# Kernel tuning notes

Hardware: AMD Instinct MI355X
Metric: run time of the kernel (lower is better)

Reference implementation:

```python
import jax, jax.numpy as jnp
import numpy as np

N = 50000        # nodes
E = 800000       # edges per edge set (avg degree 16)
IN_DIM = 128
NHID = 128
OUT_DIM = 64


def _dgcn(x, ei, w=None):
    # DGCNConv: symmetric-normalized weighted scatter-add (no self loops, no learned weight)
    src, dst = ei[0], ei[1]
    ww = jnp.ones(src.shape[0], x.dtype) if w is None else w
    deg = jax.ops.segment_sum(ww, src, num_segments=N)
    dinv = jnp.where(deg > 0, jax.lax.rsqrt(jnp.maximum(deg, 1e-30)), 0.0)
    norm = dinv[src] * ww * dinv[dst]                    # [E]
    return jax.ops.segment_sum(x[src] * norm[:, None], dst, num_segments=N)


def _digcn(x, W, b, ei, w):
    # DIGCNConv: x @ W then edge-weighted scatter-add (weights precomputed), + bias
    xw = x @ W                                           # [N, out]
    src, dst = ei[0], ei[1]
    agg = jax.ops.segment_sum(xw[src] * w[:, None], dst, num_segments=N)
    return agg + b


def setup_inputs() -> dict:
    key = jax.random.key(0)
    ks = jax.random.split(key, 32)
    def edges(k):
        return jax.random.randint(k, (2, E), 0, N, dtype=jnp.int32)
    def w(k, shape, s=0.05):
        return jax.random.normal(k, shape, dtype=jnp.float32) * s
    inp = {
        "x": jax.random.normal(ks[0], (N, IN_DIM), dtype=jnp.float32),
        "edge_index": edges(ks[1]),
        "edge_in": edges(ks[2]),
        "in_w": jax.random.uniform(ks[3], (E,), dtype=jnp.float32),
        "edge_out": edges(ks[4]),
        "out_w": jax.random.uniform(ks[5], (E,), dtype=jnp.float32),
        "edge_index_ib": edges(ks[6]),
        "edge_weight_ib": jax.random.uniform(ks[7], (E,), dtype=jnp.float32),
        "edge_index2_ib": edges(ks[8]),
        "edge_weight2_ib": jax.random.uniform(ks[9], (E,), dtype=jnp.float32),
        # lin1 / lin2 (no bias), torch Linear convention W: [out, in]
        "lin1_w": w(ks[10], (NHID, IN_DIM)),
        "lin2_w": w(ks[11], (OUT_DIM, NHID)),
        # InceptionBlock 1: Linear(in->nhid) + two DIGCNConv(in->nhid)
        "ib1_ln_w": w(ks[12], (NHID, IN_DIM)),
        "ib1_ln_b": w(ks[13], (NHID,)),
        "ib1_c1_w": w(ks[14], (IN_DIM, NHID)),
        "ib1_c1_b": w(ks[15], (NHID,)),
        "ib1_c2_w": w(ks[16], (IN_DIM, NHID)),
        "ib1_c2_b": w(ks[17], (NHID,)),
        # InceptionBlock 2: nhid -> nhid
        "ib2_ln_w": w(ks[18], (NHID, NHID)),
        "ib2_ln_b": w(ks[19], (NHID,)),
        "ib2_c1_w": w(ks[20], (NHID, NHID)),
        "ib2_c1_b": w(ks[21], (NHID,)),
        "ib2_c2_w": w(ks[22], (NHID, NHID)),
        "ib2_c2_b": w(ks[23], (NHID,)),
        # Conv1d(2*nhid -> nhid, k=1) == pointwise linear: [nhid, 2*nhid]
        "conv1_w": w(ks[24], (NHID, 2 * NHID)),
        "conv1_b": w(ks[25], (NHID,)),
    }
    return inp


def reference(x, edge_index, edge_in, in_w, edge_out, out_w,
              edge_index_ib, edge_weight_ib, edge_index2_ib, edge_weight2_ib,
              lin1_w, lin2_w,
              ib1_ln_w, ib1_ln_b, ib1_c1_w, ib1_c1_b, ib1_c2_w, ib1_c2_b,
              ib2_ln_w, ib2_ln_b, ib2_c1_w, ib2_c1_b, ib2_c2_w, ib2_c2_b,
              conv1_w, conv1_b):
    # --- sym branch 1 (uses original sym edge_index) ---
    symx = x @ lin1_w.T
    symx = (_dgcn(symx, edge_index)
            + _dgcn(symx, edge_in, in_w)
            + _dgcn(symx, edge_out, out_w))
    # --- InceptionBlock 1 ---
    x0 = x @ ib1_ln_w.T + ib1_ln_b
    x1 = _digcn(x, ib1_c1_w, ib1_c1_b, edge_index_ib, edge_weight_ib)
    x2 = _digcn(x, ib1_c2_w, ib1_c2_b, edge_index2_ib, edge_weight2_ib)
    h = x0 + x1 + x2
    # cat + Conv1d(k=1) + relu  (dropout = identity in eval mode)
    h = jnp.concatenate([h, symx], axis=-1)              # [N, 2*nhid]
    h = jax.nn.relu(h @ conv1_w.T + conv1_b)
    # --- InceptionBlock 2 ---
    x0 = h @ ib2_ln_w.T + ib2_ln_b
    x1 = _digcn(h, ib2_c1_w, ib2_c1_b, edge_index_ib, edge_weight_ib)
    x2 = _digcn(h, ib2_c2_w, ib2_c2_b, edge_index2_ib, edge_weight2_ib)
    h = jax.nn.relu(x0 + x1 + x2)
    # --- final sym branch: NOTE edge_index was reassigned to edge_index_tuple[0] ---
    symx = h @ lin2_w.T
    out = (_dgcn(symx, edge_index_ib)
           + _dgcn(symx, edge_in, in_w)
           + _dgcn(symx, edge_out, out_w))
    return out
```

## Files before the change

### kernel.cpp

```cpp
#include <hip/hip_runtime.h>


static inline int cdiv(int a, int b) { return (a + b - 1) / b; }

struct __align__(8) TmpE { ushort s, d; float w; };

using bf16x8 = __attribute__((ext_vector_type(8))) short;
using f32x4  = __attribute__((ext_vector_type(4))) float;

constexpr int NCH  = 64;
constexpr int NCHH = 32;
constexpr int NW   = 25600;
constexpr int RNG  = 25000;
constexpr int AGS  = 384;

__device__ __forceinline__ float b2f(uint u)  { return __uint_as_float(u << 16); }
__device__ __forceinline__ float b2fh(uint u) { return __uint_as_float(u & 0xFFFF0000u); }
__device__ __forceinline__ ushort f2b(float f) {
  uint u = __float_as_uint(f);
  return (ushort)((u + 0x7FFFu + ((u >> 16) & 1u)) >> 16);
}
__device__ __forceinline__ uint pk2(float a, float b) {
  return (uint)f2b(a) | ((uint)f2b(b) << 16);
}
__device__ __forceinline__ uint pkent(uint s, float w) {
  return s | ((uint)f2b(w) << 16);
}


struct HistArgs {
  const int* ik[2];
  const int* fk[2]; const float* fw[2];
  uint* pint; float* pf32; int N, CH, E;
};

__global__ __launch_bounds__(1024) void k_hist(HistArgs a) {
  const int y = blockIdx.y, chunk = blockIdx.x;
  __shared__ uint h[NW];
  int e1 = min(a.E, (chunk + 1) * a.CH);
  if (y < 2) {
    const int* __restrict__ key = a.ik[y];
    for (int i = threadIdx.x; i < NW; i += 1024) h[i] = 0;
    __syncthreads();
    for (int e = chunk * a.CH + threadIdx.x; e < e1; e += 1024) {
      uint idx = (uint)key[e];
      atomicAdd(&h[idx >> 1], 1u << ((idx & 1) << 4));
    }
    __syncthreads();
    uint* out = a.pint + ((size_t)y * NCHH + chunk) * NW;
    for (int i = threadIdx.x; i < NW; i += 1024) out[i] = h[i];
  } else {
    const int job = (y - 2) >> 1, range = (y - 2) & 1;
    const int* __restrict__ key = a.fk[job];
    const float* __restrict__ w = a.fw[job];
    float* hf = (float*)h;
    for (int i = threadIdx.x; i < RNG; i += 1024) hf[i] = 0.0f;
    __syncthreads();
    const int base = range * RNG, hi = min(a.N, base + RNG);
    for (int e = chunk * a.CH + threadIdx.x; e < e1; e += 1024) {
      int s = key[e];
      if (s >= base && s < hi) atomicAdd(&hf[s - base], w[e]);
    }
    __syncthreads();
    float* out = a.pf32 + ((size_t)job * NCHH + chunk) * a.N;
    for (int i = threadIdx.x; i < hi - base; i += 1024) out[base + i] = hf[i];
  }
}


struct B1Jobs { const int* src[5]; const int* dst[5]; const float* w[5]; };

__global__ __launch_bounds__(256) void k_b1count(B1Jobs jobs, uint* __restrict__ bcnt,
                                                 int CH, int E) {
  const int chunk = blockIdx.x, set = blockIdx.y;
  const int* __restrict__ dst = jobs.dst[set];
  __shared__ uint h[256];
  h[threadIdx.x] = 0;
  __syncthreads();
  int e1 = min(E, (chunk + 1) * CH);
  for (int e = chunk * CH + threadIdx.x; e < e1; e += 256)
    atomicAdd(&h[((uint)dst[e]) >> 8], 1u);
  __syncthreads();
  bcnt[((size_t)set * NCH + chunk) * 256 + threadIdx.x] = h[threadIdx.x];
}

__global__ __launch_bounds__(1024) void k_scanfin(
    const uint* __restrict__ bcnt, uint* __restrict__ bpos, uint* __restrict__ bbase,
    const uint* __restrict__ pint, const float* __restrict__ pf32,
    float* __restrict__ dinv, int N, int E) {
  if (blockIdx.y == 0) {
    if (blockIdx.x >= 5) return;
    const int set = blockIdx.x;
    constexpr int CELLS = NCH * 256;
    constexpr int PER = CELLS / 1024;
    __shared__ uint lds[CELLS];
    __shared__ uint psum[1024];
    for (int i = threadIdx.x; i < CELLS; i += 1024) {
      int b = i / NCH, c = i % NCH;
      lds[i] = bcnt[((size_t)set * NCH + c) * 256 + b];
    }
    __syncthreads();
    uint s = 0;
#pragma unroll
    for (int k = 0; k < PER; k++) s += lds[threadIdx.x * PER + k];
    psum[threadIdx.x] = s;
    __syncthreads();
    for (int d = 1; d < 1024; d <<= 1) {
      uint t = (threadIdx.x >= d) ? psum[threadIdx.x - d] : 0;
      __syncthreads();
      psum[threadIdx.x] += t;
      __syncthreads();
    }
    uint run = threadIdx.x ? psum[threadIdx.x - 1] : 0;
#pragma unroll
    for (int k = 0; k < PER; k++) {
      uint v = lds[threadIdx.x * PER + k];
      lds[threadIdx.x * PER + k] = run;
      run += v;
    }
    __syncthreads();
    for (int i = threadIdx.x; i < CELLS; i += 1024) {
      int b = i / NCH, c = i % NCH;
      bpos[((size_t)set * NCH + c) * 256 + b] = lds[i];
      if (c == 0) bbase[(size_t)set * 257 + b] = lds[i];
    }
    if (threadIdx.x == 0) bbase[(size_t)set * 257 + 256] = (uint)E;
  } else {
    int n = blockIdx.x * 1024 + threadIdx.x;
    if (n >= N) return;
    const int wd = n >> 1, sh = (n & 1) << 4;
    uint s_sym = 0, s_ib = 0;
    float din = 0.0f, dout = 0.0f;
#pragma unroll
    for (int c = 0; c < NCHH; c++) {
      s_sym += (pint[((size_t)0 * NCHH + c) * NW + wd] >> sh) & 0xFFFFu;
      s_ib  += (pint[((size_t)1 * NCHH + c) * NW + wd] >> sh) & 0xFFFFu;
      din   += pf32[((size_t)0 * NCHH + c) * N + n];
      dout  += pf32[((size_t)1 * NCHH + c) * N + n];
    }
    dinv[(size_t)0 * N + n] = s_sym ? rsqrtf((float)s_sym) : 0.0f;
    dinv[(size_t)1 * N + n] = din  > 0.0f ? rsqrtf(din)  : 0.0f;
    dinv[(size_t)2 * N + n] = dout > 0.0f ? rsqrtf(dout) : 0.0f;
    dinv[(size_t)3 * N + n] = s_ib ? rsqrtf((float)s_ib) : 0.0f;
  }
}

__global__ __launch_bounds__(256) void k_b1scatter(B1Jobs jobs, const uint* __restrict__ bpos,
                                                   TmpE* __restrict__ tmp, int CH, int E) {
  const int chunk = blockIdx.x, set = blockIdx.y;
  const int* __restrict__ src = jobs.src[set];
  const int* __restrict__ dst = jobs.dst[set];
  const float* __restrict__ w = jobs.w[set];
  TmpE* __restrict__ tset = tmp + (size_t)set * E;
  __shared__ uint cur[256];
  cur[threadIdx.x] = bpos[((size_t)set * NCH + chunk) * 256 + threadIdx.x];
  __syncthreads();
  int e1 = min(E, (chunk + 1) * CH);
  for (int e = chunk * CH + threadIdx.x; e < e1; e += 256) {
    uint d = (uint)dst[e];
    uint pos = atomicAdd(&cur[d >> 8], 1u);
    TmpE t;
    t.s = (ushort)src[e];
    t.d = (ushort)d;
    t.w = w ? w[e] : 1.0f;
    tset[pos] = t;
  }
}


struct B2Job { const float* dinv; uint* entA; uint* entB; int raw; };
struct B2Jobs { B2Job j[5]; };

struct PrepArgs {
  const float *x; ushort *xb; int nx;
  const float *ln, *c1, *c2, *lin1, *convw; ushort *Wf1;
  const float *lnb, *c1b, *c2b, *convb; float *Bf1;
  const float *ln2, *c12, *c22; ushort *Wst2;
  const float *ln2b, *c1b2, *c2b2; float *bias2;
  const float *lin2; ushort *Wlin2;
};

__global__ __launch_bounds__(256) void k_b2prep(
    B2Jobs jobs, const TmpE* __restrict__ tmp, const uint* __restrict__ bbase,
    int* __restrict__ rptr, int N, int E, int NBK, PrepArgs a) {
  const int y = blockIdx.y;
  if (y < 5) {
    if (blockIdx.x >= NBK) return;
    const int b = blockIdx.x, set = y;
    const B2Job jb = jobs.j[set];
    const TmpE* __restrict__ tset = tmp + (size_t)set * E;
    const uint base = bbase[(size_t)set * 257 + b];
    const uint end  = bbase[(size_t)set * 257 + b + 1];
    __shared__ uint cnt[256];
    __shared__ uint scn[256];
    cnt[threadIdx.x] = 0;
    __syncthreads();
    for (uint t = base + threadIdx.x; t < end; t += 256)
      atomicAdd(&cnt[tset[t].d & 255], 1u);
    __syncthreads();
    uint v = cnt[threadIdx.x];
    scn[threadIdx.x] = v;
    __syncthreads();
    for (int d = 1; d < 256; d <<= 1) {
      uint t2 = (threadIdx.x >= d) ? scn[threadIdx.x - d] : 0;
      __syncthreads();
      scn[threadIdx.x] += t2;
      __syncthreads();
    }
    const uint ex = scn[threadIdx.x] - v;
    const int node0 = b << 8;
    int* rp = rptr + (size_t)set * (N + 1);
    if (node0 + threadIdx.x < N) rp[node0 + threadIdx.x] = (int)(base + ex);
    if (b == 0 && threadIdx.x == 0) rp[N] = (int)bbase[(size_t)set * 257 + 256];
    __syncthreads();
    cnt[threadIdx.x] = base + ex;
    __syncthreads();
    for (uint t = base + threadIdx.x; t < end; t += 256) {
      TmpE e = tset[t];
      uint pos = atomicAdd(&cnt[e.d & 255], 1u);
      float wA = jb.raw ? e.w : jb.dinv[e.s] * e.w * jb.dinv[e.d];
      jb.entA[pos] = pkent(e.s, wA);
      if (jb.entB) jb.entB[pos] = pkent(e.s, jb.dinv[e.s] * jb.dinv[e.d]);
    }
  } else if (y == 5) {
    int i = (blockIdx.x * 256 + threadIdx.x) * 16;
    if (i < a.nx) {
#pragma unroll
      for (int q = 0; q < 4; q++) {
        float4 v = *reinterpret_cast<const float4*>(a.x + i + q * 4);
        ushort4 o;
        o.x = f2b(v.x); o.y = f2b(v.y); o.z = f2b(v.z); o.w = f2b(v.w);
        *reinterpret_cast<ushort4*>(a.xb + i + q * 4) = o;
      }
    }
  } else {
    const int x = blockIdx.x;
    if (x < 256) {
      int id = x * 256 + threadIdx.x;
      int m = id >> 9, k = id & 511;
      int p = k >> 7, kk = k & 127;
      float s = 0.0f;
      if (p == 0) {
        for (int j = 0; j < 128; j++) s = fmaf(a.ln[j * 128 + kk], a.convw[m * 256 + j], s);
      } else if (p == 1) {
        for (int j = 0; j < 128; j++) s = fmaf(a.c1[kk * 128 + j], a.convw[m * 256 + j], s);
      } else if (p == 2) {
        for (int j = 0; j < 128; j++) s = fmaf(a.c2[kk * 128 + j], a.convw[m * 256 + j], s);
      } else {
        for (int j = 0; j < 128; j++) s = fmaf(a.lin1[j * 128 + kk], a.convw[m * 256 + 128 + j], s);
      }
      a.Wf1[m * 512 + k] = f2b(s);
    } else if (x < 448) {
      int id = (x - 256) * 256 + threadIdx.x;
      int m = id / 384, k = id % 384;
      int p = k >> 7, kk = k & 127;
      float v = (p == 0) ? a.ln2[m * 128 + kk]
              : (p == 1) ? a.c12[kk * 128 + m] : a.c22[kk * 128 + m];
      a.Wst2[m * 384 + k] = f2b(v);
    } else if (x < 456) {
      int i = ((x - 448) * 256 + threadIdx.x) * 4;
      if (i < 64 * 128) {
        float4 v = *reinterpret_cast<const float4*>(a.lin2 + i);
        ushort4 o;
        o.x = f2b(v.x); o.y = f2b(v.y); o.z = f2b(v.z); o.w = f2b(v.w);
        *reinterpret_cast<ushort4*>(a.Wlin2 + i) = o;
      }
    } else if (x == 456) {
      if (threadIdx.x < 128) {
        int m = threadIdx.x;
        float s = a.convb[m];
        for (int j = 0; j < 128; j++)
          s = fmaf(a.lnb[j] + a.c1b[j] + a.c2b[j], a.convw[m * 256 + j], s);
        a.Bf1[m] = s;
      }
    } else if (x == 457) {
      if (threadIdx.x < 128)
        a.bias2[threadIdx.x] = a.ln2b[threadIdx.x] + a.c1b2[threadIdx.x] + a.c2b2[threadIdx.x];
    }
  }
}

template <int K, int K1, int LDA2, int BN, bool RELU>
__global__ __launch_bounds__(256) void k_mgemm(
    const ushort* A1, const ushort* A2,
    const ushort* __restrict__ Wt, const float* __restrict__ bias,
    ushort* C, int N) {
  constexpr int WAVES_N = BN / 64;
  constexpr int WAVES_M = 4 / WAVES_N;
  constexpr int TM = 64 / WAVES_M;
  constexpr int MF = TM / 16;
  constexpr int NF = 4;

  const int tid = threadIdx.x;
  const int wid = tid >> 6;
  const int lane = tid & 63;
  const int lr = lane & 15;
  const int g = lane >> 4;
  const int wm = wid / WAVES_N;
  const int wnn = wid % WAVES_N;
  const int row0 = blockIdx.x * 64 + wm * TM;
  const int col0 = wnn * 64;

  f32x4 acc[MF][NF];
#pragma unroll
  for (int mi = 0; mi < MF; mi++)
#pragma unroll
    for (int ni = 0; ni < NF; ni++)
#pragma unroll
      for (int r = 0; r < 4; r++) acc[mi][ni][r] = 0.0f;

#pragma unroll
  for (int kk = 0; kk < K / 32; kk++) {
    const ushort* A; int lda, kofs;
    if (kk * 32 < K1) { A = A1; lda = 128; kofs = kk * 32; }
    else              { A = A2; lda = LDA2; kofs = kk * 32 - K1; }
    bf16x8 af[MF], bfr[NF];
#pragma unroll
    for (int mi = 0; mi < MF; mi++)
      af[mi] = *reinterpret_cast<const bf16x8*>(
          A + (size_t)(row0 + mi * 16 + lr) * lda + kofs + 8 * g);
#pragma unroll
    for (int ni = 0; ni < NF; ni++)
      bfr[ni] = *reinterpret_cast<const bf16x8*>(
          Wt + (size_t)(col0 + ni * 16 + lr) * K + kk * 32 + 8 * g);
#pragma unroll
    for (int mi = 0; mi < MF; mi++)
#pragma unroll
      for (int ni = 0; ni < NF; ni++)
        acc[mi][ni] = __builtin_amdgcn_mfma_f32_16x16x32_bf16(
            af[mi], bfr[ni], acc[mi][ni], 0, 0, 0);
  }

  float bv[NF];
#pragma unroll
  for (int ni = 0; ni < NF; ni++) bv[ni] = bias ? bias[col0 + ni * 16 + lr] : 0.0f;

#pragma unroll
  for (int mi = 0; mi < MF; mi++)
#pragma unroll
    for (int r = 0; r < 4; r++) {
      int row = row0 + mi * 16 + g * 4 + r;
      if (row >= N) continue;
#pragma unroll
      for (int ni = 0; ni < NF; ni++) {
        float v = acc[mi][ni][r] + bv[ni];
        if (RELU) v = fmaxf(v, 0.0f);
        C[(size_t)row * BN + col0 + ni * 16 + lr] = f2b(v);
      }
    }
}

__global__ __launch_bounds__(256) void k_mgemm23(
    const ushort* A1, const ushort* A2,
    const ushort* __restrict__ Wt, const float* __restrict__ bias,
    const ushort* __restrict__ W2, ushort* __restrict__ B64, int N) {
  constexpr int K = 384, K1 = 128;
  const int tid = threadIdx.x;
  const int wid = tid >> 6;
  const int lane = tid & 63;
  const int lr = lane & 15;
  const int g = lane >> 4;
  const int wm = wid >> 1;
  const int wnn = wid & 1;
  const int brow = blockIdx.x * 64;
  const int row0 = brow + wm * 32;
  const int col0 = wnn * 64;

  __shared__ ushort h2t[64][136];

  f32x4 acc[2][4];
#pragma unroll
  for (int mi = 0; mi < 2; mi++)
#pragma unroll
    for (int ni = 0; ni < 4; ni++)
#pragma unroll
      for (int r = 0; r < 4; r++) acc[mi][ni][r] = 0.0f;

#pragma unroll
  for (int kk = 0; kk < K / 32; kk++) {
    const ushort* A; int lda, kofs;
    if (kk * 32 < K1) { A = A1; lda = 128; kofs = kk * 32; }
    else              { A = A2; lda = AGS; kofs = kk * 32 - K1; }
    bf16x8 af[2], bfr[4];
#pragma unroll
    for (int mi = 0; mi < 2; mi++)
      af[mi] = *reinterpret_cast<const bf16x8*>(
          A + (size_t)(row0 + mi * 16 + lr) * lda + kofs + 8 * g);
#pragma unroll
    for (int ni = 0; ni < 4; ni++)
      bfr[ni] = *reinterpret_cast<const bf16x8*>(
          Wt + (size_t)(col0 + ni * 16 + lr) * K + kk * 32 + 8 * g);
#pragma unroll
    for (int mi = 0; mi < 2; mi++)
#pragma unroll
      for (int ni = 0; ni < 4; ni++)
        acc[mi][ni] = __builtin_amdgcn_mfma_f32_16x16x32_bf16(
            af[mi], bfr[ni], acc[mi][ni], 0, 0, 0);
  }

  float bv[4];
#pragma unroll
  for (int ni = 0; ni < 4; ni++) bv[ni] = bias[col0 + ni * 16 + lr];

#pragma unroll
  for (int mi = 0; mi < 2; mi++)
#pragma unroll
    for (int r = 0; r < 4; r++) {
      int lrow = wm * 32 + mi * 16 + g * 4 + r;
#pragma unroll
      for (int ni = 0; ni < 4; ni++)
        h2t[lrow][col0 + ni * 16 + lr] = f2b(fmaxf(acc[mi][ni][r] + bv[ni], 0.0f));
    }
  __syncthreads();

  f32x4 a2[4];
#pragma unroll
  for (int ni = 0; ni < 4; ni++)
#pragma unroll
    for (int r = 0; r < 4; r++) a2[ni][r] = 0.0f;
  const int prow = wid * 16;
#pragma unroll
  for (int kk = 0; kk < 4; kk++) {
    bf16x8 af = *reinterpret_cast<const bf16x8*>(&h2t[prow + lr][kk * 32 + 8 * g]);
#pragma unroll
    for (int ni = 0; ni < 4; ni++) {
      bf16x8 bf = *reinterpret_cast<const bf16x8*>(
          W2 + (size_t)(ni * 16 + lr) * 128 + kk * 32 + 8 * g);
      a2[ni] = __builtin_amdgcn_mfma_f32_16x16x32_bf16(af, bf, a2[ni], 0, 0, 0);
    }
  }
#pragma unroll
  for (int r = 0; r < 4; r++) {
    int row = brow + prow + g * 4 + r;
    if (row >= N) continue;
#pragma unroll
    for (int ni = 0; ni < 4; ni++)
      B64[(size_t)row * 64 + ni * 16 + lr] = f2b(a2[ni][r]);
  }
}


#define GLD(P) (*reinterpret_cast<const uint4*>(X + (size_t)((P) & 0xFFFFu) * 128 + l * 8))

#define GFMA(P, V)                                                \
  {                                                               \
    float _w = b2fh(P);                                           \
    c0 = fmaf(_w, b2f(V.x), c0);  c1 = fmaf(_w, b2fh(V.x), c1);   \
    c2 = fmaf(_w, b2f(V.y), c2);  c3 = fmaf(_w, b2fh(V.y), c3);   \
    c4 = fmaf(_w, b2f(V.z), c4);  c5 = fmaf(_w, b2fh(V.z), c5);   \
    c6 = fmaf(_w, b2f(V.w), c6);  c7 = fmaf(_w, b2fh(V.w), c7);   \
  }

#define GLOOP(rp, ee, X)                                                              \
  {                                                                                   \
    int i = rp[row], en = rp[row + 1];                                                \
    for (; i + 8 <= en; i += 8) {                                                     \
      uint p0 = ee[i],     p1 = ee[i + 1], p2 = ee[i + 2], p3 = ee[i + 3];            \
      uint p4 = ee[i + 4], p5 = ee[i + 5], p6 = ee[i + 6], p7 = ee[i + 7];            \
      uint4 v0 = GLD(p0), v1 = GLD(p1), v2 = GLD(p2), v3 = GLD(p3);                   \
      uint4 v4 = GLD(p4), v5 = GLD(p5), v6 = GLD(p6), v7 = GLD(p7);                   \
      GFMA(p0, v0); GFMA(p1, v1); GFMA(p2, v2); GFMA(p3, v3);                         \
      GFMA(p4, v4); GFMA(p5, v5); GFMA(p6, v6); GFMA(p7, v7);                         \
    }                                                                                 \
    for (; i + 4 <= en; i += 4) {                                                     \
      uint p0 = ee[i], p1 = ee[i + 1], p2 = ee[i + 2], p3 = ee[i + 3];                \
      uint4 v0 = GLD(p0), v1 = GLD(p1), v2 = GLD(p2), v3 = GLD(p3);                   \
      GFMA(p0, v0); GFMA(p1, v1); GFMA(p2, v2); GFMA(p3, v3);                         \
    }                                                                                 \
    for (; i < en; ++i) {                                                             \
      uint p0 = ee[i];                                                                \
      uint4 v0 = GLD(p0);                                                             \
      GFMA(p0, v0);                                                                   \
    }                                                                                 \
  }

#define PK8() make_uint4(pk2(c0, c1), pk2(c2, c3), pk2(c4, c5), pk2(c6, c7))
#define ZACC() c0 = c1 = c2 = c3 = c4 = c5 = c6 = c7 = 0.0f

__global__ __launch_bounds__(256) void k_gather_s1(
    const ushort* __restrict__ X, ushort* __restrict__ AG,
    const int* __restrict__ rp_ib,  const uint* __restrict__ e_ib,
    const int* __restrict__ rp_ib2, const uint* __restrict__ e_ib2,
    const int* __restrict__ rp_sym, const uint* __restrict__ e_sym,
    const int* __restrict__ rp_in,  const uint* __restrict__ e_in,
    const int* __restrict__ rp_out, const uint* __restrict__ e_out,
    int N) {
  int row = blockIdx.x * 16 + (threadIdx.x >> 4);
  if (row >= N) return;
  int l = threadIdx.x & 15;
  uint4* o = reinterpret_cast<uint4*>(AG + (size_t)row * AGS + l * 8);
  float c0, c1, c2, c3, c4, c5, c6, c7;
  if (blockIdx.y == 0) {
    ZACC();
    GLOOP(rp_ib, e_ib, X);
    o[0] = PK8();
    ZACC();
    GLOOP(rp_ib2, e_ib2, X);
    o[16] = PK8();
  } else {
    ZACC();
    GLOOP(rp_sym, e_sym, X);
    GLOOP(rp_in,  e_in,  X);
    GLOOP(rp_out, e_out, X);
    o[32] = PK8();
  }
}

__global__ __launch_bounds__(256) void k_gather_s2(
    const ushort* __restrict__ X, ushort* __restrict__ AG,
    const int* __restrict__ rp_ib,  const uint* __restrict__ e_ib,
    const int* __restrict__ rp_ib2, const uint* __restrict__ e_ib2,
    int N) {
  int row = blockIdx.x * 16 + (threadIdx.x >> 4);
  if (row >= N) return;
  int l = threadIdx.x & 15;
  uint4* o = reinterpret_cast<uint4*>(AG + (size_t)row * AGS + l * 8);
  float c0, c1, c2, c3, c4, c5, c6, c7;
  if (blockIdx.y == 0) {
    ZACC();
    GLOOP(rp_ib, e_ib, X);
    o[0] = PK8();
  } else {
    ZACC();
    GLOOP(rp_ib2, e_ib2, X);
    o[16] = PK8();
  }
}

#define OLD2(P) (*reinterpret_cast<const uint2*>(X + (size_t)((P) & 0xFFFFu) * 64 + l * 4))
#define OFMA(P, V)                                                 \
  {                                                                \
    float _w = b2fh(P);                                            \
    a0 = fmaf(_w, b2f(V.x), a0);  a1 = fmaf(_w, b2fh(V.x), a1);    \
    a2 = fmaf(_w, b2f(V.y), a2);  a3 = fmaf(_w, b2fh(V.y), a3);    \
  }

__global__ __launch_bounds__(256) void k_gather_out(
    const ushort* __restrict__ X, float* __restrict__ out,
    const int* __restrict__ rp0, const uint* __restrict__ e0,
    const int* __restrict__ rp1, const uint* __restrict__ e1,
    const int* __restrict__ rp2, const uint* __restrict__ e2,
    int N) {
  int row = blockIdx.x * 16 + (threadIdx.x >> 4);
  if (row >= N) return;
  int l = threadIdx.x & 15;
  float a0 = 0, a1 = 0, a2 = 0, a3 = 0;
  auto loop = [&](const int* __restrict__ rp, const uint* __restrict__ ee) {
    int i = rp[row], en = rp[row + 1];
    for (; i + 8 <= en; i += 8) {
      uint p0 = ee[i],     p1 = ee[i + 1], p2 = ee[i + 2], p3 = ee[i + 3];
      uint p4 = ee[i + 4], p5 = ee[i + 5], p6 = ee[i + 6], p7 = ee[i + 7];
      uint2 v0 = OLD2(p0), v1 = OLD2(p1), v2 = OLD2(p2), v3 = OLD2(p3);
      uint2 v4 = OLD2(p4), v5 = OLD2(p5), v6 = OLD2(p6), v7 = OLD2(p7);
      OFMA(p0, v0); OFMA(p1, v1); OFMA(p2, v2); OFMA(p3, v3);
      OFMA(p4, v4); OFMA(p5, v5); OFMA(p6, v6); OFMA(p7, v7);
    }
    for (; i + 4 <= en; i += 4) {
      uint p0 = ee[i], p1 = ee[i + 1], p2 = ee[i + 2], p3 = ee[i + 3];
      uint2 v0 = OLD2(p0), v1 = OLD2(p1), v2 = OLD2(p2), v3 = OLD2(p3);
      OFMA(p0, v0); OFMA(p1, v1); OFMA(p2, v2); OFMA(p3, v3);
    }
    for (; i < en; ++i) {
      uint p0 = ee[i];
      uint2 v0 = OLD2(p0);
      OFMA(p0, v0);
    }
  };
  loop(rp0, e0); loop(rp1, e1); loop(rp2, e2);
  *reinterpret_cast<float4*>(out + (size_t)row * 64 + l * 4) =
      make_float4(a0, a1, a2, a3);
}


extern "C" void kernel_launch(void* const* d_in, const int* in_sizes, int n_in,
                              void* d_out, int out_size, void* d_ws, size_t ws_size,
                              hipStream_t stream) {
  const float* x        = (const float*)d_in[0];
  const int*   ei_sym   = (const int*)d_in[1];
  const int*   ei_in    = (const int*)d_in[2];
  const float* in_w     = (const float*)d_in[3];
  const int*   ei_out   = (const int*)d_in[4];
  const float* out_w    = (const float*)d_in[5];
  const int*   ei_ib    = (const int*)d_in[6];
  const float* w_ib     = (const float*)d_in[7];
  const int*   ei_ib2   = (const int*)d_in[8];
  const float* w_ib2    = (const float*)d_in[9];
  const float* lin1_w   = (const float*)d_in[10];
  const float* lin2_w   = (const float*)d_in[11];
  const float* ib1_ln_w = (const float*)d_in[12];
  const float* ib1_ln_b = (const float*)d_in[13];
  const float* ib1_c1_w = (const float*)d_in[14];
  const float* ib1_c1_b = (const float*)d_in[15];
  const float* ib1_c2_w = (const float*)d_in[16];
  const float* ib1_c2_b = (const float*)d_in[17];
  const float* ib2_ln_w = (const float*)d_in[18];
  const float* ib2_ln_b = (const float*)d_in[19];
  const float* ib2_c1_w = (const float*)d_in[20];
  const float* ib2_c1_b = (const float*)d_in[21];
  const float* ib2_c2_w = (const float*)d_in[22];
  const float* ib2_c2_b = (const float*)d_in[23];
  const float* conv1_w  = (const float*)d_in[24];
  const float* conv1_b  = (const float*)d_in[25];

  const int N = in_sizes[0] / 128;
  const int E = in_sizes[1] / 2;
  const int CHB = cdiv(E, NCH);
  const int CHH = cdiv(E, NCHH);
  const int NBK = cdiv(N, 256);

  size_t off = 0;
  auto alloc = [&](size_t bytes) -> void* {
    void* p = (char*)d_ws + off;
    off = (off + bytes + 255) & ~size_t(255);
    return p;
  };
  ushort* xb = (ushort*)alloc((size_t)N * 128 * 2);
  ushort* AG = (ushort*)alloc((size_t)N * AGS * 2);
  ushort* BH = (ushort*)alloc((size_t)N * 128 * 2);
  ushort* B64 = (ushort*)alloc((size_t)N * 64 * 2);
  TmpE*  tmp  = (TmpE*)AG;
  float* pf32 = (float*)BH;
  uint*  pint = (uint*)alloc(2 * (size_t)NCHH * NW * 4);
  uint* ent_sym = (uint*)alloc((size_t)E * 4);
  uint* ent_in  = (uint*)alloc((size_t)E * 4);
  uint* ent_out = (uint*)alloc((size_t)E * 4);
  uint* ent_ibr = (uint*)alloc((size_t)E * 4);
  uint* ent_ibn = (uint*)alloc((size_t)E * 4);
  uint* ent_ib2 = (uint*)alloc((size_t)E * 4);
  int*  rptr = (int*)alloc(5 * (size_t)(N + 1) * 4);
  float* dinv = (float*)alloc(4 * (size_t)N * 4);
  uint* bcnt  = (uint*)alloc(5 * (size_t)NCH * 256 * 4);
  uint* bpos  = (uint*)alloc(5 * (size_t)NCH * 256 * 4);
  uint* bbase = (uint*)alloc(5 * 257 * 4);
  ushort* Wf1   = (ushort*)alloc(128 * 512 * 2);
  ushort* Wst2  = (ushort*)alloc(128 * 384 * 2);
  ushort* Wb_lin2 = (ushort*)alloc(64 * 128 * 2);
  float* Bf1   = (float*)alloc(128 * 4);
  float* bias2 = (float*)alloc(128 * 4);

  const int TB = 256;
  const int gM = cdiv(N, 64);
  const int gR16 = cdiv(N, 16);

  const int* rp_sym = rptr + 0 * (N + 1);
  const int* rp_in  = rptr + 1 * (N + 1);
  const int* rp_out = rptr + 2 * (N + 1);
  const int* rp_ib  = rptr + 3 * (N + 1);
  const int* rp_ib2 = rptr + 4 * (N + 1);

  {
    HistArgs ha;
    ha.ik[0] = ei_sym; ha.ik[1] = ei_ib;
    ha.fk[0] = ei_in;  ha.fw[0] = in_w;
    ha.fk[1] = ei_out; ha.fw[1] = out_w;
    ha.pint = pint; ha.pf32 = pf32; ha.N = N; ha.CH = CHH; ha.E = E;
    k_hist<<<dim3(NCHH, 6), 1024, 0, stream>>>(ha);
  }

  B1Jobs bj;
  bj.src[0] = ei_sym; bj.dst[0] = ei_sym + E; bj.w[0] = nullptr;
  bj.src[1] = ei_in;  bj.dst[1] = ei_in + E;  bj.w[1] = in_w;
  bj.src[2] = ei_out; bj.dst[2] = ei_out + E; bj.w[2] = out_w;
  bj.src[3] = ei_ib;  bj.dst[3] = ei_ib + E;  bj.w[3] = w_ib;
  bj.src[4] = ei_ib2; bj.dst[4] = ei_ib2 + E; bj.w[4] = w_ib2;
  k_b1count<<<dim3(NCH, 5), 256, 0, stream>>>(bj, bcnt, CHB, E);

  k_scanfin<<<dim3(cdiv(N, 1024), 2), 1024, 0, stream>>>(
      bcnt, bpos, bbase, pint, pf32, dinv, N, E);

  k_b1scatter<<<dim3(NCH, 5), 256, 0, stream>>>(bj, bpos, tmp, CHB, E);

  {
    B2Jobs j2;
    j2.j[0] = { dinv + 0 * N, ent_sym, nullptr, 0 };
    j2.j[1] = { dinv + 1 * N, ent_in,  nullptr, 0 };
    j2.j[2] = { dinv + 2 * N, ent_out, nullptr, 0 };
    j2.j[3] = { dinv + 3 * N, ent_ibr, ent_ibn, 1 };
    j2.j[4] = { nullptr,      ent_ib2, nullptr, 1 };
    PrepArgs pa;
    pa.x = x; pa.xb = xb; pa.nx = N * 128;
    pa.ln = ib1_ln_w; pa.c1 = ib1_c1_w; pa.c2 = ib1_c2_w; pa.lin1 = lin1_w;
    pa.convw = conv1_w; pa.Wf1 = Wf1;
    pa.lnb = ib1_ln_b; pa.c1b = ib1_c1_b; pa.c2b = ib1_c2_b; pa.convb = conv1_b;
    pa.Bf1 = Bf1;
    pa.ln2 = ib2_ln_w; pa.c12 = ib2_c1_w; pa.c22 = ib2_c2_w; pa.Wst2 = Wst2;
    pa.ln2b = ib2_ln_b; pa.c1b2 = ib2_c1_b; pa.c2b2 = ib2_c2_b; pa.bias2 = bias2;
    pa.lin2 = lin2_w; pa.Wlin2 = Wb_lin2;
    int gx = max(cdiv(N * 128, TB * 16), 458);
    k_b2prep<<<dim3(gx, 7), TB, 0, stream>>>(j2, tmp, bbase, rptr, N, E, NBK, pa);
  }

  k_gather_s1<<<dim3(gR16, 2), TB, 0, stream>>>(xb, AG, rp_ib, ent_ibr, rp_ib2, ent_ib2,
                                                rp_sym, ent_sym, rp_in, ent_in,
                                                rp_out, ent_out, N);
  k_mgemm<512, 128, AGS, 128, true><<<gM, TB, 0, stream>>>(xb, AG, Wf1, Bf1, BH, N);

  k_gather_s2<<<dim3(gR16, 2), TB, 0, stream>>>(BH, AG, rp_ib, ent_ibr, rp_ib2, ent_ib2, N);
  k_mgemm23<<<gM, TB, 0, stream>>>(BH, AG, Wst2, bias2, Wb_lin2, B64, N);

  k_gather_out<<<gR16, TB, 0, stream>>>(B64, (float*)d_out,
                                        rp_ib, ent_ibn, rp_in, ent_in, rp_out, ent_out, N);
}
```

Measured before the change: 459.1 us.

## Gather first-stage features from FP8 copy of x and merge histogram/count kernels

Adds an FP8 (e4m3) copy of the input features alongside the bf16 one and makes the first-stage neighbor gather read 8 bytes per lane instead of 16, halving the gathered bytes for the five edge sets. It also folds the per-bucket destination count kernel into the histogram kernel as extra grid rows, removing one launch. FP8 quantization of x lowers the precision of the aggregated features, which may loosen accuracy against the reference.

```diff
diff --git a/kernel.cpp b/kernel.cpp
--- a/kernel.cpp
+++ b/kernel.cpp
@@ -7,6 +7,7 @@
 
 using bf16x8 = __attribute__((ext_vector_type(8))) short;
 using f32x4  = __attribute__((ext_vector_type(4))) float;
+using f32x2  = __attribute__((ext_vector_type(2))) float;
 
 constexpr int NCH  = 64;
 constexpr int NCHH = 32;
@@ -28,28 +29,32 @@
 }
 
 
-struct HistArgs {
+struct HCArgs {
   const int* ik[2];
   const int* fk[2]; const float* fw[2];
-  uint* pint; float* pf32; int N, CH, E;
+  const int* cdst[5];
+  uint* pint; float* pf32; uint* bcnt;
+  int N, CHH, CHB, E;
 };
 
-__global__ __launch_bounds__(1024) void k_hist(HistArgs a) {
+__global__ __launch_bounds__(1024) void k_histcnt(HCArgs a) {
   const int y = blockIdx.y, chunk = blockIdx.x;
   __shared__ uint h[NW];
-  int e1 = min(a.E, (chunk + 1) * a.CH);
   if (y < 2) {
+    if (chunk >= NCHH) return;
     const int* __restrict__ key = a.ik[y];
     for (int i = threadIdx.x; i < NW; i += 1024) h[i] = 0;
     __syncthreads();
-    for (int e = chunk * a.CH + threadIdx.x; e < e1; e += 1024) {
+    int e1 = min(a.E, (chunk + 1) * a.CHH);
+    for (int e = chunk * a.CHH + threadIdx.x; e < e1; e += 1024) {
       uint idx = (uint)key[e];
       atomicAdd(&h[idx >> 1], 1u << ((idx & 1) << 4));
     }
     __syncthreads();
     uint* out = a.pint + ((size_t)y * NCHH + chunk) * NW;
     for (int i = threadIdx.x; i < NW; i += 1024) out[i] = h[i];
-  } else {
+  } else if (y < 6) {
+    if (chunk >= NCHH) return;
     const int job = (y - 2) >> 1, range = (y - 2) & 1;
     const int* __restrict__ key = a.fk[job];
     const float* __restrict__ w = a.fw[job];
@@ -57,31 +62,26 @@
     for (int i = threadIdx.x; i < RNG; i += 1024) hf[i] = 0.0f;
     __syncthreads();
     const int base = range * RNG, hi = min(a.N, base + RNG);
-    for (int e = chunk * a.CH + threadIdx.x; e < e1; e += 1024) {
+    int e1 = min(a.E, (chunk + 1) * a.CHH);
+    for (int e = chunk * a.CHH + threadIdx.x; e < e1; e += 1024) {
       int s = key[e];
       if (s >= base && s < hi) atomicAdd(&hf[s - base], w[e]);
     }
     __syncthreads();
     float* out = a.pf32 + ((size_t)job * NCHH + chunk) * a.N;
     for (int i = threadIdx.x; i < hi - base; i += 1024) out[base + i] = hf[i];
-  }
-}
-
-
-struct B1Jobs { const int* src[5]; const int* dst[5]; const float* w[5]; };
-
-__global__ __launch_bounds__(256) void k_b1count(B1Jobs jobs, uint* __restrict__ bcnt,
-                                                 int CH, int E) {
-  const int chunk = blockIdx.x, set = blockIdx.y;
-  const int* __restrict__ dst = jobs.dst[set];
-  __shared__ uint h[256];
-  h[threadIdx.x] = 0;
-  __syncthreads();
-  int e1 = min(E, (chunk + 1) * CH);
-  for (int e = chunk * CH + threadIdx.x; e < e1; e += 256)
-    atomicAdd(&h[((uint)dst[e]) >> 8], 1u);
-  __syncthreads();
-  bcnt[((size_t)set * NCH + chunk) * 256 + threadIdx.x] = h[threadIdx.x];
+  } else {
+    const int set = y - 6;
+    const int* __restrict__ dst = a.cdst[set];
+    if (threadIdx.x < 256) h[threadIdx.x] = 0;
+    __syncthreads();
+    int e1 = min(a.E, (chunk + 1) * a.CHB);
+    for (int e = chunk * a.CHB + threadIdx.x; e < e1; e += 1024)
+      atomicAdd(&h[((uint)dst[e]) >> 8], 1u);
+    __syncthreads();
+    if (threadIdx.x < 256)
+      a.bcnt[((size_t)set * NCH + chunk) * 256 + threadIdx.x] = h[threadIdx.x];
+  }
 }
 
 __global__ __launch_bounds__(1024) void k_scanfin(
@@ -144,6 +144,8 @@
     dinv[(size_t)3 * N + n] = s_ib ? rsqrtf((float)s_ib) : 0.0f;
   }
 }
+
+struct B1Jobs { const int* src[5]; const int* dst[5]; const float* w[5]; };
 
 __global__ __launch_bounds__(256) void k_b1scatter(B1Jobs jobs, const uint* __restrict__ bpos,
                                                    TmpE* __restrict__ tmp, int CH, int E) {
@@ -172,7 +174,7 @@
 struct B2Jobs { B2Job j[5]; };
 
 struct PrepArgs {
-  const float *x; ushort *xb; int nx;
+  const float *x; ushort *xb; uchar *xb8; int nx;
   const float *ln, *c1, *c2, *lin1, *convw; ushort *Wf1;
   const float *lnb, *c1b, *c2b, *convb; float *Bf1;
   const float *ln2, *c12, *c22; ushort *Wst2;
@@ -225,13 +227,20 @@
   } else if (y == 5) {
     int i = (blockIdx.x * 256 + threadIdx.x) * 16;
     if (i < a.nx) {
+      uint4 p8;
+      uint* p8w = (uint*)&p8;
 #pragma unroll
       for (int q = 0; q < 4; q++) {
         float4 v = *reinterpret_cast<const float4*>(a.x + i + q * 4);
         ushort4 o;
         o.x = f2b(v.x); o.y = f2b(v.y); o.z = f2b(v.z); o.w = f2b(v.w);
         *reinterpret_cast<ushort4*>(a.xb + i + q * 4) = o;
+        int w8 = 0;
+        w8 = __builtin_amdgcn_cvt_pk_fp8_f32(v.x, v.y, w8, false);
+        w8 = __builtin_amdgcn_cvt_pk_fp8_f32(v.z, v.w, w8, true);
+        p8w[q] = (uint)w8;
       }
+      *reinterpret_cast<uint4*>(a.xb8 + i) = p8;
     }
   } else {
     const int x = blockIdx.x;
@@ -440,6 +449,77 @@
 }
 
 
+#define GLD8(P) (*reinterpret_cast<const uint2*>(X8 + (size_t)((P) & 0xFFFFu) * 128 + l * 8))
+
+#define GFMA8(P, V)                                                        \
+  {                                                                        \
+    float _w = b2fh(P);                                                    \
+    f32x2 q0 = __builtin_amdgcn_cvt_pk_f32_fp8((int)V.x, false);           \
+    f32x2 q1 = __builtin_amdgcn_cvt_pk_f32_fp8((int)V.x, true);            \
+    f32x2 q2 = __builtin_amdgcn_cvt_pk_f32_fp8((int)V.y, false);           \
+    f32x2 q3 = __builtin_amdgcn_cvt_pk_f32_fp8((int)V.y, true);            \
+    c0 = fmaf(_w, q0.x, c0);  c1 = fmaf(_w, q0.y, c1);                     \
+    c2 = fmaf(_w, q1.x, c2);  c3 = fmaf(_w, q1.y, c3);                     \
+    c4 = fmaf(_w, q2.x, c4);  c5 = fmaf(_w, q2.y, c5);                     \
+    c6 = fmaf(_w, q3.x, c6);  c7 = fmaf(_w, q3.y, c7);                     \
+  }
+
+#define GLOOP8(rp, ee)                                                                \
+  {                                                                                   \
+    int i = rp[row], en = rp[row + 1];                                                \
+    for (; i + 8 <= en; i += 8) {                                                     \
+      uint p0 = ee[i],     p1 = ee[i + 1], p2 = ee[i + 2], p3 = ee[i + 3];            \
+      uint p4 = ee[i + 4], p5 = ee[i + 5], p6 = ee[i + 6], p7 = ee[i + 7];            \
+      uint2 v0 = GLD8(p0), v1 = GLD8(p1), v2 = GLD8(p2), v3 = GLD8(p3);               \
+      uint2 v4 = GLD8(p4), v5 = GLD8(p5), v6 = GLD8(p6), v7 = GLD8(p7);               \
+      GFMA8(p0, v0); GFMA8(p1, v1); GFMA8(p2, v2); GFMA8(p3, v3);                     \
+      GFMA8(p4, v4); GFMA8(p5, v5); GFMA8(p6, v6); GFMA8(p7, v7);                     \
+    }                                                                                 \
+    for (; i + 4 <= en; i += 4) {                                                     \
+      uint p0 = ee[i], p1 = ee[i + 1], p2 = ee[i + 2], p3 = ee[i + 3];                \
+      uint2 v0 = GLD8(p0), v1 = GLD8(p1), v2 = GLD8(p2), v3 = GLD8(p3);               \
+      GFMA8(p0, v0); GFMA8(p1, v1); GFMA8(p2, v2); GFMA8(p3, v3);                     \
+    }                                                                                 \
+    for (; i < en; ++i) {                                                             \
+      uint p0 = ee[i];                                                                \
+      uint2 v0 = GLD8(p0);                                                            \
+      GFMA8(p0, v0);                                                                  \
+    }                                                                                 \
+  }
+
+#define PK8() make_uint4(pk2(c0, c1), pk2(c2, c3), pk2(c4, c5), pk2(c6, c7))
+#define ZACC() c0 = c1 = c2 = c3 = c4 = c5 = c6 = c7 = 0.0f
+
+__global__ __launch_bounds__(256) void k_gather_s1(
+    const uchar* __restrict__ X8, ushort* __restrict__ AG,
+    const int* __restrict__ rp_ib,  const uint* __restrict__ e_ib,
+    const int* __restrict__ rp_ib2, const uint* __restrict__ e_ib2,
+    const int* __restrict__ rp_sym, const uint* __restrict__ e_sym,
+    const int* __restrict__ rp_in,  const uint* __restrict__ e_in,
+    const int* __restrict__ rp_out, const uint* __restrict__ e_out,
+    int N) {
+  int row = blockIdx.x * 16 + (threadIdx.x >> 4);
+  if (row >= N) return;
+  int l = threadIdx.x & 15;
+  uint4* o = reinterpret_cast<uint4*>(AG + (size_t)row * AGS + l * 8);
+  float c0, c1, c2, c3, c4, c5, c6, c7;
+  if (blockIdx.y == 0) {
+    ZACC();
+    GLOOP8(rp_ib, e_ib);
+    o[0] = PK8();
+    ZACC();
+    GLOOP8(rp_ib2, e_ib2);
+    o[16] = PK8();
+  } else {
+    ZACC();
+    GLOOP8(rp_sym, e_sym);
+    GLOOP8(rp_in,  e_in);
+    GLOOP8(rp_out, e_out);
+    o[32] = PK8();
+  }
+}
+
+
 #define GLD(P) (*reinterpret_cast<const uint4*>(X + (size_t)((P) & 0xFFFFu) * 128 + l * 8))
 
 #define GFMA(P, V)                                                \
@@ -473,38 +553,6 @@
       GFMA(p0, v0);                                                                   \
     }                                                                                 \
   }
-
-#define PK8() make_uint4(pk2(c0, c1), pk2(c2, c3), pk2(c4, c5), pk2(c6, c7))
-#define ZACC() c0 = c1 = c2 = c3 = c4 = c5 = c6 = c7 = 0.0f
-
-__global__ __launch_bounds__(256) void k_gather_s1(
-    const ushort* __restrict__ X, ushort* __restrict__ AG,
-    const int* __restrict__ rp_ib,  const uint* __restrict__ e_ib,
-    const int* __restrict__ rp_ib2, const uint* __restrict__ e_ib2,
-    const int* __restrict__ rp_sym, const uint* __restrict__ e_sym,
-    const int* __restrict__ rp_in,  const uint* __restrict__ e_in,
-    const int* __restrict__ rp_out, const uint* __restrict__ e_out,
-    int N) {
-  int row = blockIdx.x * 16 + (threadIdx.x >> 4);
-  if (row >= N) return;
-  int l = threadIdx.x & 15;
-  uint4* o = reinterpret_cast<uint4*>(AG + (size_t)row * AGS + l * 8);
-  float c0, c1, c2, c3, c4, c5, c6, c7;
-  if (blockIdx.y == 0) {
-    ZACC();
-    GLOOP(rp_ib, e_ib, X);
-    o[0] = PK8();
-    ZACC();
-    GLOOP(rp_ib2, e_ib2, X);
-    o[16] = PK8();
-  } else {
-    ZACC();
-    GLOOP(rp_sym, e_sym, X);
-    GLOOP(rp_in,  e_in,  X);
-    GLOOP(rp_out, e_out, X);
-    o[32] = PK8();
-  }
-}
 
 __global__ __launch_bounds__(256) void k_gather_s2(
     const ushort* __restrict__ X, ushort* __restrict__ AG,
@@ -615,6 +663,7 @@
     return p;
   };
   ushort* xb = (ushort*)alloc((size_t)N * 128 * 2);
+  uchar*  xb8 = (uchar*)alloc((size_t)N * 128);
   ushort* AG = (ushort*)alloc((size_t)N * AGS * 2);
   ushort* BH = (ushort*)alloc((size_t)N * 128 * 2);
   ushort* B64 = (ushort*)alloc((size_t)N * 64 * 2);
@@ -649,13 +698,19 @@
   const int* rp_ib2 = rptr + 4 * (N + 1);
 
   {
-    HistArgs ha;
-    ha.ik[0] = ei_sym; ha.ik[1] = ei_ib;
-    ha.fk[0] = ei_in;  ha.fw[0] = in_w;
-    ha.fk[1] = ei_out; ha.fw[1] = out_w;
-    ha.pint = pint; ha.pf32 = pf32; ha.N = N; ha.CH = CHH; ha.E = E;
-    k_hist<<<dim3(NCHH, 6), 1024, 0, stream>>>(ha);
-  }
+    HCArgs hc;
+    hc.ik[0] = ei_sym; hc.ik[1] = ei_ib;
+    hc.fk[0] = ei_in;  hc.fw[0] = in_w;
+    hc.fk[1] = ei_out; hc.fw[1] = out_w;
+    hc.cdst[0] = ei_sym + E; hc.cdst[1] = ei_in + E; hc.cdst[2] = ei_out + E;
+    hc.cdst[3] = ei_ib + E;  hc.cdst[4] = ei_ib2 + E;
+    hc.pint = pint; hc.pf32 = pf32; hc.bcnt = bcnt;
+    hc.N = N; hc.CHH = CHH; hc.CHB = CHB; hc.E = E;
+    k_histcnt<<<dim3(NCH, 11), 1024, 0, stream>>>(hc);
+  }
+
+  k_scanfin<<<dim3(cdiv(N, 1024), 2), 1024, 0, stream>>>(
+      bcnt, bpos, bbase, pint, pf32, dinv, N, E);
 
   B1Jobs bj;
   bj.src[0] = ei_sym; bj.dst[0] = ei_sym + E; bj.w[0] = nullptr;
@@ -663,11 +718,6 @@
   bj.src[2] = ei_out; bj.dst[2] = ei_out + E; bj.w[2] = out_w;
   bj.src[3] = ei_ib;  bj.dst[3] = ei_ib + E;  bj.w[3] = w_ib;
   bj.src[4] = ei_ib2; bj.dst[4] = ei_ib2 + E; bj.w[4] = w_ib2;
-  k_b1count<<<dim3(NCH, 5), 256, 0, stream>>>(bj, bcnt, CHB, E);
-
-  k_scanfin<<<dim3(cdiv(N, 1024), 2), 1024, 0, stream>>>(
-      bcnt, bpos, bbase, pint, pf32, dinv, N, E);
-
   k_b1scatter<<<dim3(NCH, 5), 256, 0, stream>>>(bj, bpos, tmp, CHB, E);
 
   {
@@ -678,7 +728,7 @@
     j2.j[3] = { dinv + 3 * N, ent_ibr, ent_ibn, 1 };
     j2.j[4] = { nullptr,      ent_ib2, nullptr, 1 };
     PrepArgs pa;
-    pa.x = x; pa.xb = xb; pa.nx = N * 128;
+    pa.x = x; pa.xb = xb; pa.xb8 = xb8; pa.nx = N * 128;
     pa.ln = ib1_ln_w; pa.c1 = ib1_c1_w; pa.c2 = ib1_c2_w; pa.lin1 = lin1_w;
     pa.convw = conv1_w; pa.Wf1 = Wf1;
     pa.lnb = ib1_ln_b; pa.c1b = ib1_c1_b; pa.c2b = ib1_c2_b; pa.convb = conv1_b;
@@ -690,7 +740,7 @@
     k_b2prep<<<dim3(gx, 7), TB, 0, stream>>>(j2, tmp, bbase, rptr, N, E, NBK, pa);
   }
 
-  k_gather_s1<<<dim3(gR16, 2), TB, 0, stream>>>(xb, AG, rp_ib, ent_ibr, rp_ib2, ent_ib2,
+  k_gather_s1<<<dim3(gR16, 2), TB, 0, stream>>>(xb8, AG, rp_ib, ent_ibr, rp_ib2, ent_ib2,
                                                 rp_sym, ent_sym, rp_in, ent_in,
                                                 rp_out, ent_out, N);
   k_mgemm<512, 128, AGS, 128, true><<<gM, TB, 0, stream>>>(xb, AG, Wf1, Bf1, BH, N);
```

Result: faster. 403.7 us (-12.1%).
